# Optimization experiments

Hardware: AMD Instinct MI355X
Metric: run time of the kernel (lower is better)

Reference implementation:

```python
import jax, jax.numpy as jnp
import numpy as np

N_CG_ITERS = 100


def _conv_same(x, k):
    # x: [C,H,W], k: [kh,kw]; depthwise cross-correlation, zero padding ('same')
    C = x.shape[0]
    rhs = jnp.broadcast_to(k, (C, 1) + k.shape)  # [C,1,kh,kw]
    return jax.lax.conv_general_dilated(
        x[None], rhs, window_strides=(1, 1), padding='SAME',
        dimension_numbers=('NCHW', 'OIHW', 'NCHW'),
        feature_group_count=C)[0]


def _flip(k):
    return k[::-1, ::-1]


def _apply_A(p, kernel, wsq, reg_kernels):
    # A = K^T K + sum_i w_i^2 G_i^T G_i
    KtKp = _conv_same(_conv_same(p, kernel), _flip(kernel))
    def one_reg(g):
        return _conv_same(_conv_same(p, g), _flip(g))
    reg = jax.vmap(one_reg)(reg_kernels)  # [n_reg, C, H, W]
    return KtKp + jnp.einsum('n,nchw->chw', wsq, reg)


def setup_inputs() -> dict:
    key = jax.random.key(0)
    k1, k2, k3, k4 = jax.random.split(key, 4)
    image = jax.random.uniform(k1, (3, 512, 512), dtype=jnp.float32)
    kernel = jax.random.uniform(k2, (11, 11), dtype=jnp.float32)
    kernel = kernel / jnp.sum(kernel)  # normalized blur PSF
    reg_kernels = 0.01 * jax.random.normal(k3, (2, 3, 3), dtype=jnp.float32)
    reg_kernel_weights = 1.0 + 0.01 * jax.random.normal(k4, (2,), dtype=jnp.float32)
    return {'image': image, 'kernel': kernel,
            'reg_kernel_weights': reg_kernel_weights, 'reg_kernels': reg_kernels}


def reference(image, kernel, reg_kernel_weights, reg_kernels):
    wsq = reg_kernel_weights * reg_kernel_weights
    # CG init: b = K^T * image, x0 = image, r0 = b - A x0, p0 = r0
    b = _conv_same(image, _flip(kernel))
    x0 = image
    r0 = b - _apply_A(x0, kernel, wsq, reg_kernels)
    p0 = r0

    def cg_step(carry, _):
        x, r, p = carry
        Ap = _apply_A(p, kernel, wsq, reg_kernels)
        rTr = jnp.sum(r * r)
        alpha = rTr / jnp.sum(p * Ap)
        x_new = x + alpha * p
        r_new = r - alpha * Ap
        beta = jnp.sum(r_new * r_new) / rTr
        p_new = r_new + beta * p
        return (x_new, r_new, p_new), None

    (x, r, p), _ = jax.lax.scan(cg_step, (x0, r0, p0), None, length=N_CG_ITERS)
    return x  # xrp[0] -> solved image [C,H,W]
```

## Files before the change

kernel.cpp:

```cpp
#include <hip/hip_runtime.h>


static constexpr int H = 512, W = 512, CCH = 3;
static constexpr int NPIX = CCH * H * W;
static constexpr int TDIM = 64;
static constexpr int RAD = 5;
static constexpr int HALO = 10;
static constexpr int PR = TDIM + 2 * HALO;
static constexpr int PSTR = PR + 1;
static constexpr int TR = TDIM + 2 * RAD;
static constexpr int TSTR = TR + 1;
static constexpr int NBLK = CCH * 8 * 8;
static constexpr int NTHR = 512;
static constexpr int NITER = 100;

__device__ __forceinline__ float block_reduce0(float v, float* red, int tid)
{
    __syncthreads();
    #pragma unroll
    for (int m = 32; m; m >>= 1) v += __shfl_xor(v, m, 64);
    if ((tid & 63) == 0) red[tid >> 6] = v;
    __syncthreads();
    float s = 0.f;
    if (tid == 0) {
        #pragma unroll
        for (int i = 0; i < NTHR / 64; ++i) s += red[i];
    }
    return s;
}

__device__ __forceinline__ float allreduce_bar(unsigned long long* slots, unsigned seq,
                                               float thread_partial,
                                               float* red, float* bc, int tid, int bid)
{
    float part = block_reduce0(thread_partial, red, tid);
    asm volatile("s_waitcnt vmcnt(0)" ::: "memory");
    __syncthreads();
    unsigned long long* buf = slots + (size_t)(seq & 1u) * 256;
    if (tid == 0) {
        unsigned long long u = ((unsigned long long)seq << 32)
                             | (unsigned long long)__float_as_uint(part);
        __hip_atomic_store(&buf[bid], u, __ATOMIC_RELAXED, __HIP_MEMORY_SCOPE_AGENT);
    }
    float mine = 0.f;
    if (tid < NBLK) {
        unsigned long long v;
        for (;;) {
            v = __hip_atomic_load(&buf[tid], __ATOMIC_RELAXED, __HIP_MEMORY_SCOPE_AGENT);
            if ((unsigned)(v >> 32) == seq) break;
            __builtin_amdgcn_s_sleep(1);
        }
        mine = __uint_as_float((unsigned)v);
    }
    float s = block_reduce0(mine, red, tid);
    if (tid == 0) *bc = s;
    __syncthreads();
    return *bc;
}

__device__ __forceinline__ void conv_fwd_phase(const float* __restrict__ kern,
                                               const float* __restrict__ P_,
                                               float* __restrict__ T_,
                                               int by0, int bx0, int tid)
{
    for (int seg = tid; seg < TR * 10; seg += NTHR) {
        int ry  = seg / 10;
        int rx0 = (seg - ry * 10) << 3;
        int gy  = by0 - RAD + ry;
        bool rowIn = (gy >= 0 && gy < H);
        float acc[8];
        #pragma unroll
        for (int j = 0; j < 8; ++j) acc[j] = 0.f;
        for (int a = 0; a < 11; ++a) {
            const float* row = P_ + (ry + a) * PSTR + rx0;
            float v[18];
            #pragma unroll
            for (int b = 0; b < 18; ++b) v[b] = row[b];
            #pragma unroll
            for (int b = 0; b < 11; ++b) {
                float kw = kern[a * 11 + b];
                #pragma unroll
                for (int j = 0; j < 8; ++j) acc[j] = fmaf(v[b + j], kw, acc[j]);
            }
        }
        #pragma unroll
        for (int j = 0; j < 8; ++j) {
            int rx = rx0 + j;
            if (rx < TR) {
                int gx = bx0 - RAD + rx;
                bool in = rowIn && gx >= 0 && gx < W;
                T_[ry * TSTR + rx] = in ? acc[j] : 0.f;
            }
        }
    }
}

__device__ __forceinline__ void conv11_flip_acc(const float* __restrict__ src, int stride,
                                                int row0, int col0,
                                                const float* __restrict__ kern,
                                                float acc[8])
{
    for (int a = 0; a < 11; ++a) {
        const float* row = src + (row0 + a) * stride + col0;
        float v[18];
        #pragma unroll
        for (int b = 0; b < 18; ++b) v[b] = row[b];
        #pragma unroll
        for (int b = 0; b < 11; ++b) {
            float kw = kern[(10 - a) * 11 + (10 - b)];
            #pragma unroll
            for (int j = 0; j < 8; ++j) acc[j] = fmaf(v[b + j], kw, acc[j]);
        }
    }
}

__device__ __forceinline__ void reg_acc(const float* __restrict__ P_,
                                        const float* __restrict__ CB_,
                                        const float* __restrict__ gk,
                                        float w0sq, float w1sq,
                                        int oy, int ox0, int gy, int gx0,
                                        float acc[8])
{
    bool interior = (gy >= 1 && gy < H - 1 && gx0 >= 1 && gx0 <= W - 9);
    if (interior) {
        for (int a = 0; a < 5; ++a) {
            const float* row = P_ + (oy + 8 + a) * PSTR + ox0 + 8;
            float v[12];
            #pragma unroll
            for (int b = 0; b < 12; ++b) v[b] = row[b];
            #pragma unroll
            for (int b = 0; b < 5; ++b) {
                float cb = CB_[a * 5 + b];
                #pragma unroll
                for (int j = 0; j < 8; ++j) acc[j] = fmaf(v[b + j], cb, acc[j]);
            }
        }
    } else {
        for (int j = 0; j < 8; ++j) {
            int gx = gx0 + j;
            float racc = 0.f;
            for (int dy = -1; dy <= 1; ++dy)
                for (int dx = -1; dx <= 1; ++dx) {
                    int qy = gy + dy, qx = gx + dx;
                    if (qy >= 0 && qy < H && qx >= 0 && qx < W) {
                        float u0 = 0.f, u1 = 0.f;
                        int pr0 = oy + 10 + dy - 1, pc0 = ox0 + j + 10 + dx - 1;
                        for (int sy = 0; sy < 3; ++sy)
                            for (int sx = 0; sx < 3; ++sx) {
                                float pv = P_[(pr0 + sy) * PSTR + pc0 + sx];
                                u0 = fmaf(pv, gk[sy * 3 + sx], u0);
                                u1 = fmaf(pv, gk[9 + sy * 3 + sx], u1);
                            }
                        racc += w0sq * gk[(1 - dy) * 3 + (1 - dx)] * u0
                              + w1sq * gk[9 + (1 - dy) * 3 + (1 - dx)] * u1;
                    }
                }
            acc[j] += racc;
        }
    }
}

__global__ void slot_init(unsigned long long* slots) { slots[threadIdx.x] = 0ull; }

__global__ void __launch_bounds__(NTHR)
deconv_cg(const float* __restrict__ img, const float* __restrict__ kern,
          const float* __restrict__ wts, const float* __restrict__ gk,
          float* __restrict__ out, float* __restrict__ ws)
{
    __shared__ float P[PR * PSTR + 32];
    __shared__ float T[TR * TSTR + 32];
    __shared__ float CB[25];
    __shared__ float red[NTHR / 64];
    __shared__ float bc;

    const int tid = threadIdx.x;
    const int bid = blockIdx.x;
    const int ch  = bid / 64;
    const int tt  = bid - ch * 64;
    const int by0 = (tt >> 3) * TDIM;
    const int bx0 = (tt & 7) * TDIM;

    const float* imgc = img + ch * H * W;
    unsigned long long* slots = (unsigned long long*)ws;
    unsigned long long* Hg    = (unsigned long long*)ws + 512;
    unsigned long long* Hc    = Hg + (size_t)ch * H * W;

    const float w0 = wts[0], w1 = wts[1];
    const float w0sq = w0 * w0, w1sq = w1 * w1;

    if (tid < 25) {
        int ty = tid / 5 - 2, tx = tid % 5 - 2;
        float s = 0.f;
        for (int ay = 0; ay < 3; ++ay)
            for (int ax = 0; ax < 3; ++ax) {
                int by_ = ay + ty, bx_ = ax + tx;
                if (by_ >= 0 && by_ < 3 && bx_ >= 0 && bx_ < 3)
                    s += w0sq * gk[ay * 3 + ax] * gk[by_ * 3 + bx_]
                       + w1sq * gk[9 + ay * 3 + ax] * gk[9 + by_ * 3 + bx_];
            }
        CB[tid] = s;
    }

    const int oy  = tid >> 3;
    const int ox0 = (tid & 7) << 3;
    const int gy  = by0 + oy;
    const int gx0 = bx0 + ox0;
    bool strip[8];
    #pragma unroll
    for (int j = 0; j < 8; ++j) {
        int ox = ox0 + j;
        strip[j] = (oy < HALO) | (oy >= TDIM - HALO) | (ox < HALO) | (ox >= TDIM - HALO);
    }

    float xr[8], rr[8], pr[8];

    for (int idx = tid; idx < PR * PR; idx += NTHR) {
        int py = idx / PR, px = idx - py * PR;
        int iy = by0 - HALO + py, ix = bx0 - HALO + px;
        float v = 0.f;
        if (iy >= 0 && iy < H && ix >= 0 && ix < W) v = imgc[iy * W + ix];
        P[py * PSTR + px] = v;
    }
    __syncthreads();
    conv_fwd_phase(kern, P, T, by0, bx0, tid);
    __syncthreads();
    float rTr, beta = 0.f;
    {
        float accA[8], accB[8];
        #pragma unroll
        for (int j = 0; j < 8; ++j) { accA[j] = 0.f; accB[j] = 0.f; }
        conv11_flip_acc(T, TSTR, oy, ox0, kern, accA);
        conv11_flip_acc(P, PSTR, oy + 5, ox0 + 5, kern, accB);
        reg_acc(P, CB, gk, w0sq, w1sq, oy, ox0, gy, gx0, accA);
        float dr = 0.f;
        #pragma unroll
        for (int j = 0; j < 8; ++j) {
            float r0 = accB[j] - accA[j];
            rr[j] = r0;
            pr[j] = r0;
            xr[j] = P[(oy + HALO) * PSTR + ox0 + HALO + j];
            if (strip[j]) {
                unsigned long long u = (unsigned long long)__float_as_uint(r0)
                                     | ((unsigned long long)__float_as_uint(r0) << 32);
                __hip_atomic_store(&Hc[gy * W + gx0 + j], u,
                                   __ATOMIC_RELAXED, __HIP_MEMORY_SCOPE_AGENT);
            }
            dr = fmaf(r0, r0, dr);
        }
        rTr = allreduce_bar(slots, 1u, dr, red, &bc, tid, bid);
    }

    for (int it = 0; it < NITER; ++it) {
        #pragma unroll
        for (int j = 0; j < 8; ++j) pr[j] = fmaf(beta, pr[j], rr[j]);
        for (int idx = tid; idx < PR * PR; idx += NTHR) {
            int py = idx / PR, px = idx - py * PR;
            if (py >= HALO && py < HALO + TDIM && px >= HALO && px < HALO + TDIM)
                continue;
            int iy = by0 - HALO + py, ix = bx0 - HALO + px;
            float v = 0.f;
            if (iy >= 0 && iy < H && ix >= 0 && ix < W) {
                unsigned long long u = __hip_atomic_load(&Hc[iy * W + ix],
                                       __ATOMIC_RELAXED, __HIP_MEMORY_SCOPE_AGENT);
                float hr = __uint_as_float((unsigned)u);
                float hp = __uint_as_float((unsigned)(u >> 32));
                v = fmaf(beta, hp, hr);
            }
            P[py * PSTR + px] = v;
        }
        #pragma unroll
        for (int j = 0; j < 8; ++j)
            P[(oy + HALO) * PSTR + ox0 + HALO + j] = pr[j];
        __syncthreads();

        conv_fwd_phase(kern, P, T, by0, bx0, tid);
        __syncthreads();

        float Ap[8];
        float dp = 0.f;
        {
            float acc[8];
            #pragma unroll
            for (int j = 0; j < 8; ++j) acc[j] = 0.f;
            conv11_flip_acc(T, TSTR, oy, ox0, kern, acc);
            reg_acc(P, CB, gk, w0sq, w1sq, oy, ox0, gy, gx0, acc);
            #pragma unroll
            for (int j = 0; j < 8; ++j) {
                Ap[j] = acc[j];
                dp = fmaf(pr[j], Ap[j], dp);
            }
        }
        float pAp   = allreduce_bar(slots, 2u * it + 2u, dp, red, &bc, tid, bid);
        float alpha = rTr / pAp;

        float dr = 0.f;
        #pragma unroll
        for (int j = 0; j < 8; ++j) {
            xr[j] = fmaf(alpha, pr[j], xr[j]);
            rr[j] = fmaf(-alpha, Ap[j], rr[j]);
            if (strip[j]) {
                unsigned long long u = (unsigned long long)__float_as_uint(rr[j])
                                     | ((unsigned long long)__float_as_uint(pr[j]) << 32);
                __hip_atomic_store(&Hc[gy * W + gx0 + j], u,
                                   __ATOMIC_RELAXED, __HIP_MEMORY_SCOPE_AGENT);
            }
            dr = fmaf(rr[j], rr[j], dr);
        }
        float s = allreduce_bar(slots, 2u * it + 3u, dr, red, &bc, tid, bid);
        beta = s / rTr;
        rTr  = s;
    }

    float* outc = out + ch * H * W;
    #pragma unroll
    for (int j = 0; j < 8; ++j) outc[gy * W + gx0 + j] = xr[j];
}

extern "C" void kernel_launch(void* const* d_in, const int* in_sizes, int n_in,
                              void* d_out, int out_size, void* d_ws, size_t ws_size,
                              hipStream_t stream)
{
    (void)in_sizes; (void)n_in; (void)out_size; (void)ws_size;
    const float* img  = (const float*)d_in[0];
    const float* kern = (const float*)d_in[1];
    const float* wts  = (const float*)d_in[2];
    const float* gk   = (const float*)d_in[3];
    float* out = (float*)d_out;
    float* ws  = (float*)d_ws;

    slot_init<<<1, 512, 0, stream>>>((unsigned long long*)ws);
    deconv_cg<<<dim3(NBLK), dim3(NTHR), 0, stream>>>(img, kern, wts, gk, out, ws);
}
```

Measured before the change: 4.832 ms.

## Keep halo p locally and exchange only r values with precomputed coalesced indices

Each block now keeps its own copy of the halo search direction in a shared-memory frame buffer and updates it as p = r + beta*p_old. Only 32-bit residual values go through the global halo exchange, where the old code packed 64-bit (r,p) pairs. Boundary strip writes are staged through shared memory so that all threads issue contiguous stores, and per-thread load/store indices are precomputed once instead of being recomputed with divisions every iteration. The cost is extra shared memory, one added barrier per iteration, and a correctness dependence on the local p copy staying consistent with the neighbours' values.

```diff
diff --git a/kernel.cpp b/kernel.cpp
--- a/kernel.cpp
+++ b/kernel.cpp
@@ -13,6 +13,8 @@
 static constexpr int NBLK = CCH * 8 * 8;
 static constexpr int NTHR = 512;
 static constexpr int NITER = 100;
+static constexpr int FRN = 2960;
+static constexpr int SPN = 2160;
 
 __device__ __forceinline__ float block_reduce0(float v, float* red, int tid)
 {
@@ -167,8 +169,9 @@
           const float* __restrict__ wts, const float* __restrict__ gk,
           float* __restrict__ out, float* __restrict__ ws)
 {
-    __shared__ float P[PR * PSTR + 32];
+    __shared__ float P[PR * PSTR];
     __shared__ float T[TR * TSTR + 32];
+    __shared__ float F[FRN];
     __shared__ float CB[25];
     __shared__ float red[NTHR / 64];
     __shared__ float bc;
@@ -182,8 +185,8 @@
 
     const float* imgc = img + ch * H * W;
     unsigned long long* slots = (unsigned long long*)ws;
-    unsigned long long* Hg    = (unsigned long long*)ws + 512;
-    unsigned long long* Hc    = Hg + (size_t)ch * H * W;
+    float* Hr = ws + 1024;
+    float* Hc = Hr + (size_t)ch * H * W;
 
     const float w0 = wts[0], w1 = wts[1];
     const float w0sq = w0 * w0, w1sq = w1 * w1;
@@ -205,14 +208,44 @@
     const int ox0 = (tid & 7) << 3;
     const int gy  = by0 + oy;
     const int gx0 = bx0 + ox0;
-    bool strip[8];
+
+    int fP[6], fG[6];
     #pragma unroll
-    for (int j = 0; j < 8; ++j) {
-        int ox = ox0 + j;
-        strip[j] = (oy < HALO) | (oy >= TDIM - HALO) | (ox < HALO) | (ox >= TDIM - HALO);
+    for (int k = 0; k < 6; ++k) {
+        int idx = tid + k * NTHR;
+        fP[k] = -1; fG[k] = -1;
+        if (idx < FRN) {
+            int py, px;
+            if (idx < 840)       { py = idx / 84;              px = idx - py * 84; }
+            else if (idx < 1680) { int t = idx - 840;  py = 74 + t / 84; px = t - (t / 84) * 84; }
+            else                 { int t = idx - 1680; py = 10 + t / 20;
+                                   int c = t - (t / 20) * 20;  px = (c < 10) ? c : (c + 64); }
+            int iy = by0 - HALO + py, ix = bx0 - HALO + px;
+            if (iy >= 0 && iy < H && ix >= 0 && ix < W) {
+                fP[k] = py * PSTR + px;
+                fG[k] = iy * W + ix;
+            }
+        }
+    }
+    int pT[5], pG[5];
+    #pragma unroll
+    for (int k = 0; k < 5; ++k) {
+        int idx = tid + k * NTHR;
+        pT[k] = -1; pG[k] = 0;
+        if (idx < SPN) {
+            int sy, sx;
+            if (idx < 640)       { sy = idx >> 6;              sx = idx & 63; }
+            else if (idx < 1280) { int t = idx - 640;  sy = 54 + (t >> 6); sx = t & 63; }
+            else                 { int t = idx - 1280; sy = 10 + t / 20;
+                                   int c = t - (t / 20) * 20;  sx = (c < 10) ? c : (c + 44); }
+            pT[k] = sy * TSTR + sx;
+            pG[k] = (by0 + sy) * W + bx0 + sx;
+        }
     }
 
     float xr[8], rr[8], pr[8];
+
+    for (int idx = tid; idx < FRN; idx += NTHR) F[idx] = 0.f;
 
     for (int idx = tid; idx < PR * PR; idx += NTHR) {
         int py = idx / PR, px = idx - py * PR;
@@ -236,38 +269,39 @@
         #pragma unroll
         for (int j = 0; j < 8; ++j) {
             float r0 = accB[j] - accA[j];
-            rr[j] = r0;
-            pr[j] = r0;
+            rr[j] = r0;  pr[j] = r0;
             xr[j] = P[(oy + HALO) * PSTR + ox0 + HALO + j];
-            if (strip[j]) {
-                unsigned long long u = (unsigned long long)__float_as_uint(r0)
-                                     | ((unsigned long long)__float_as_uint(r0) << 32);
-                __hip_atomic_store(&Hc[gy * W + gx0 + j], u,
+            dr = fmaf(r0, r0, dr);
+        }
+        __syncthreads();
+        #pragma unroll
+        for (int j = 0; j < 8; ++j) T[oy * TSTR + ox0 + j] = rr[j];
+        __syncthreads();
+        #pragma unroll
+        for (int k = 0; k < 5; ++k)
+            if (pT[k] >= 0)
+                __hip_atomic_store(&Hc[pG[k]], T[pT[k]],
                                    __ATOMIC_RELAXED, __HIP_MEMORY_SCOPE_AGENT);
-            }
-            dr = fmaf(r0, r0, dr);
-        }
         rTr = allreduce_bar(slots, 1u, dr, red, &bc, tid, bid);
     }
 
     for (int it = 0; it < NITER; ++it) {
         #pragma unroll
         for (int j = 0; j < 8; ++j) pr[j] = fmaf(beta, pr[j], rr[j]);
-        for (int idx = tid; idx < PR * PR; idx += NTHR) {
-            int py = idx / PR, px = idx - py * PR;
-            if (py >= HALO && py < HALO + TDIM && px >= HALO && px < HALO + TDIM)
-                continue;
-            int iy = by0 - HALO + py, ix = bx0 - HALO + px;
-            float v = 0.f;
-            if (iy >= 0 && iy < H && ix >= 0 && ix < W) {
-                unsigned long long u = __hip_atomic_load(&Hc[iy * W + ix],
-                                       __ATOMIC_RELAXED, __HIP_MEMORY_SCOPE_AGENT);
-                float hr = __uint_as_float((unsigned)u);
-                float hp = __uint_as_float((unsigned)(u >> 32));
-                v = fmaf(beta, hp, hr);
-            }
-            P[py * PSTR + px] = v;
-        }
+        float fv[6];
+        #pragma unroll
+        for (int k = 0; k < 6; ++k)
+            fv[k] = (fG[k] >= 0)
+                  ? __hip_atomic_load(&Hc[fG[k]], __ATOMIC_RELAXED, __HIP_MEMORY_SCOPE_AGENT)
+                  : 0.f;
+        #pragma unroll
+        for (int k = 0; k < 6; ++k)
+            if (fG[k] >= 0) {
+                int fi = tid + k * NTHR;
+                float f = fmaf(beta, F[fi], fv[k]);
+                F[fi] = f;
+                P[fP[k]] = f;
+            }
         #pragma unroll
         for (int j = 0; j < 8; ++j)
             P[(oy + HALO) * PSTR + ox0 + HALO + j] = pr[j];
@@ -298,14 +332,15 @@
         for (int j = 0; j < 8; ++j) {
             xr[j] = fmaf(alpha, pr[j], xr[j]);
             rr[j] = fmaf(-alpha, Ap[j], rr[j]);
-            if (strip[j]) {
-                unsigned long long u = (unsigned long long)__float_as_uint(rr[j])
-                                     | ((unsigned long long)__float_as_uint(pr[j]) << 32);
-                __hip_atomic_store(&Hc[gy * W + gx0 + j], u,
+            T[oy * TSTR + ox0 + j] = rr[j];
+            dr = fmaf(rr[j], rr[j], dr);
+        }
+        __syncthreads();
+        #pragma unroll
+        for (int k = 0; k < 5; ++k)
+            if (pT[k] >= 0)
+                __hip_atomic_store(&Hc[pG[k]], T[pT[k]],
                                    __ATOMIC_RELAXED, __HIP_MEMORY_SCOPE_AGENT);
-            }
-            dr = fmaf(rr[j], rr[j], dr);
-        }
         float s = allreduce_bar(slots, 2u * it + 3u, dr, red, &bc, tid, bid);
         beta = s / rTr;
         rTr  = s;
```

Result: faster. 3.980 ms (-17.6%).
